# Performance work log

Measured on AMD Instinct MI355X. Metric: run time of the kernel, lower is better.

Reference implementation:

```python
import jax, jax.numpy as jnp
import numpy as np

LN_EPS = 1e-12


def layer_norm(x, g, b):
    mu = jnp.mean(x, axis=-1, keepdims=True)
    var = jnp.mean(jnp.square(x - mu), axis=-1, keepdims=True)
    return (x - mu) * jax.lax.rsqrt(var + LN_EPS) * g + b


def setup_inputs() -> dict:
    key = jax.random.key(0)
    ks = jax.random.split(key, 12)
    B, L, H, P, V = 8, 512, 768, 200, 30522
    src_scores = jax.random.normal(ks[0], (B, L, L), jnp.float32)
    seq_hidden = jax.random.normal(ks[1], (B, L, H), jnp.float32)
    seq_mask = jax.random.randint(ks[2], (B, L), 0, 2).astype(jnp.float32)
    pos_emb = jax.random.normal(ks[3], (512, P), jnp.float32) * 0.02
    Wp = jax.random.normal(ks[4], (H, P), jnp.float32) * 0.02
    bp = jnp.zeros((H,), jnp.float32)
    Wt = jax.random.normal(ks[5], (H, H), jnp.float32) * 0.02
    bt = jnp.zeros((H,), jnp.float32)
    ln_g = jnp.ones((H,), jnp.float32)
    ln_b = jnp.zeros((H,), jnp.float32)
    Wd = jax.random.normal(ks[6], (V, H), jnp.float32) * 0.02
    dec_bias = jnp.zeros((V,), jnp.float32)
    return dict(src_scores=src_scores, seq_hidden=seq_hidden, seq_mask=seq_mask,
                pos_emb=pos_emb, Wp=Wp, bp=bp, Wt=Wt, bt=bt,
                ln_g=ln_g, ln_b=ln_b, Wd=Wd, dec_bias=dec_bias)


def reference(src_scores, seq_hidden, seq_mask, pos_emb, Wp, bp, Wt, bt, ln_g, ln_b, Wd, dec_bias):
    L = src_scores.shape[1]
    # position embeddings for first L positions, projected to hidden size: [L, H]
    pos_h = pos_emb[:L] @ Wp.T + bp
    # pos_scores[b, l, s] = pos_h[l] . seq_hidden[b, s]
    pos_scores = jnp.einsum('lh,bsh->bls', pos_h, seq_hidden)
    scores = pos_scores + src_scores + seq_mask[:, None, :] * -10000.0
    alpha = jax.nn.softmax(scores, axis=-1)                 # [B, L, L]
    seq_sum = jnp.einsum('bls,bsh->blh', alpha, seq_hidden)  # [B, L, H]
    # BertPredictionHeadTransform: dense -> gelu (exact) -> LayerNorm
    h = layer_norm(jax.nn.gelu(seq_sum @ Wt.T + bt, approximate=False), ln_g, ln_b)
    target_scores = h @ Wd.T + dec_bias                      # [B, L, V]
    return target_scores
```

## Files before the change

### kernel.cpp

```cpp
#include <hip/hip_runtime.h>

using f32x4  = __attribute__((ext_vector_type(4))) float;
using short8 = __attribute__((ext_vector_type(8))) short;
using short4v= __attribute__((ext_vector_type(4))) short;
typedef __attribute__((ext_vector_type(8))) __bf16 bf16x8;

__device__ static inline short f2bf(float f){
    unsigned u = __builtin_bit_cast(unsigned, f);
    u += 0x7fffu + ((u >> 16) & 1u);
    return (short)(u >> 16);
}

__device__ static inline void gload_lds16(const void* g, void* l){
    __builtin_amdgcn_global_load_lds(
        (const __attribute__((address_space(1))) void*)g,
        (__attribute__((address_space(3))) void*)l, 16, 0, 0);
}

#define BARM() asm volatile("s_barrier" ::: "memory")

#define BKK 64

template<int EPI, bool T2D>
__global__ __launch_bounds__(256, 2)
void gemm_bt(const short* __restrict__ A, const short* __restrict__ B,
             float* __restrict__ outF, short* __restrict__ outB,
             const float* __restrict__ bias,
             const float* __restrict__ addmat, const float* __restrict__ mask,
             int K, int ldc, int Ncheck,
             long sA, long sB, long sC, long sX, int maskStride)
{
    __shared__ short Abuf[128*BKK];
    __shared__ short Bbuf[128*BKK];
    const int tid  = threadIdx.x;
    const int wave = tid >> 6;
    const int lane = tid & 63;
    const int bz   = blockIdx.z;

    int bx = blockIdx.x, by = blockIdx.y;
    if constexpr (T2D) {
        const int GX = gridDim.x, GY = gridDim.y;
        const int f  = blockIdx.y * GX + blockIdx.x;
        const int nfull  = GX >> 3;
        const int fullsz = (nfull << 3) * GY;
        int mg, mloc, nloc, nbase;
        if (f < fullsz) {
            const int band = f / (GY << 3);
            const int r    = f - band * (GY << 3);
            mg   = r >> 6;
            const int rr = r & 63;
            mloc = rr & 7; nloc = rr >> 3;
            nbase = band << 3;
        } else {
            const int rem = GX & 7;
            const int fp  = f - fullsz;
            const int gsz = rem << 3;
            mg   = fp / gsz;
            const int rr = fp - mg * gsz;
            mloc = rr & 7; nloc = rr >> 3;
            nbase = nfull << 3;
        }
        bx = nbase + nloc;
        by = (mg << 3) + mloc;
    }
    const int m0 = by * 128;
    const int n0 = bx * 128;
    const short* Ab = A + (long)bz * sA;
    const short* Bb = B + (long)bz * sB;

    const int wr = (wave >> 1) * 64;
    const int wc = (wave &  1) * 64;

    f32x4 acc[4][4];
    #pragma unroll
    for (int i=0;i<4;++i)
        #pragma unroll
        for (int j=0;j<4;++j) acc[i][j] = (f32x4){0.f,0.f,0.f,0.f};

    const int srow = wave*32 + (lane >> 3);
    const int kch  = (lane & 7) ^ (lane >> 3);
    const short* gA = Ab + (long)(m0 + srow)*K + kch*8;
    const short* gB = Bb + (long)(n0 + srow)*K + kch*8;
    short* lA = Abuf + wave*32*BKK;
    short* lB = Bbuf + wave*32*BKK;

    for (int k0 = 0; k0 < K; k0 += BKK) {
        __syncthreads();
        #pragma unroll
        for (int is=0; is<4; ++is){
            gload_lds16(gA + k0 + (long)is*8*K, lA + is*8*BKK);
            gload_lds16(gB + k0 + (long)is*8*K, lB + is*8*BKK);
        }
        __syncthreads();
        #pragma unroll
        for (int ks=0; ks<2; ++ks){
            bf16x8 af[4], bfr[4];
            const int chunk = ks*4 + (lane >> 4);
            #pragma unroll
            for (int mi=0;mi<4;++mi){
                int row = wr + mi*16 + (lane & 15);
                af[mi] = *(const bf16x8*)((const char*)Abuf + row*128 + ((chunk ^ (row & 7))<<4));
            }
            #pragma unroll
            for (int ni=0;ni<4;++ni){
                int row = wc + ni*16 + (lane & 15);
                bfr[ni] = *(const bf16x8*)((const char*)Bbuf + row*128 + ((chunk ^ (row & 7))<<4));
            }
            #pragma unroll
            for (int mi=0;mi<4;++mi)
                #pragma unroll
                for (int ni=0;ni<4;++ni)
                    acc[mi][ni] = __builtin_amdgcn_mfma_f32_16x16x32_bf16(af[mi], bfr[ni], acc[mi][ni], 0, 0, 0);
        }
    }

    const int rb = (lane >> 4) * 4;
    const int cb = lane & 15;
    #pragma unroll
    for (int mi=0;mi<4;++mi){
        #pragma unroll
        for (int r=0;r<4;++r){
            const int row = m0 + wr + mi*16 + rb + r;
            #pragma unroll
            for (int ni=0;ni<4;++ni){
                const int col = n0 + wc + ni*16 + cb;
                float v = acc[mi][ni][r];
                if constexpr (EPI == 0) {
                    v += addmat[(long)bz*sX + (long)row*ldc + col]
                         - 10000.f * mask[bz*maskStride + col];
                    outF[(long)bz*sC + (long)row*ldc + col] = v;
                } else if constexpr (EPI == 1) {
                    outB[(long)bz*sC + (long)row*ldc + col] = f2bf(v);
                } else if constexpr (EPI == 3) {
                    if (col < Ncheck) outF[(long)row*ldc + col] = v + bias[col];
                } else if constexpr (EPI == 4) {
                    outB[(long)row*ldc + col] = f2bf(v + bias[col]);
                }
            }
        }
    }
}

template<bool T2D>
__global__ __launch_bounds__(512, 1)
void gemm_bt256p(const short* __restrict__ A, const short* __restrict__ B,
                 float* __restrict__ outF, const float* __restrict__ bias,
                 int K, int ldc, int Ncheck, int maxBrow)
{
    __shared__ __align__(16) short Ab[2][2][256*32];
    __shared__ __align__(16) short Bb[2][2][256*32];
    const int tid  = threadIdx.x;
    const int wave = tid >> 6;
    const int lane = tid & 63;

    int bx = blockIdx.x, by = blockIdx.y;
    if constexpr (T2D) {
        const int GX = gridDim.x, GY = gridDim.y;
        const int f  = blockIdx.y * GX + blockIdx.x;
        const int band = f / (GY << 3);
        const int r2   = f - band * (GY << 3);
        const int mg   = r2 >> 6;
        const int rr   = r2 & 63;
        bx = (band << 3) + (rr >> 3);
        by = (mg << 3) + (rr & 7);
    }
    const int m0 = by * 256;
    const int n0 = bx * 256;

    const int wr = (wave >> 2) * 128;
    const int wc = (wave & 3) * 64;

    f32x4 acc[8][4];
    #pragma unroll
    for (int i=0;i<8;++i)
        #pragma unroll
        for (int j=0;j<4;++j) acc[i][j] = (f32x4){0.f,0.f,0.f,0.f};

    const int srow = wave*16 + (lane >> 2);
    const int cg   = (lane & 3) ^ ((lane >> 3) & 3);
    const short* gA0 = A + (long)(m0 + srow)       * K + cg*8;
    const short* gA1 = gA0 + (long)128 * K;
    int br0 = n0 + srow;        if (br0 > maxBrow) br0 = maxBrow;
    int br1 = n0 + 128 + srow;  if (br1 > maxBrow) br1 = maxBrow;
    const short* gB0 = B + (long)br0 * K + cg*8;
    const short* gB1 = B + (long)br1 * K + cg*8;
    const int so = wave*16*32;

    const int nt = K / 64;

    #define SA(bb,kh,kc) { gload_lds16(gA0 + (kc) + (kh)*32, &Ab[bb][kh][so]); \
                           gload_lds16(gA1 + (kc) + (kh)*32, &Ab[bb][kh][128*32 + so]); }
    #define SB(bb,kh,kc) { gload_lds16(gB0 + (kc) + (kh)*32, &Bb[bb][kh][so]); \
                           gload_lds16(gB1 + (kc) + (kh)*32, &Bb[bb][kh][128*32 + so]); }

    const int ch   = (lane >> 4) ^ ((lane >> 1) & 3);
    const int aoff = (wr + (lane & 15))*32 + ch*8;
    const int boff = (wc + (lane & 15))*32 + ch*8;

    SA(0,0,0); SB(0,0,0); SA(0,1,0); SB(0,1,0);
    asm volatile("s_waitcnt vmcnt(4)" ::: "memory");
    BARM();

    for (int t = 0; t < nt; ++t) {
        const int buf = t & 1, nb = buf ^ 1;
        const bool pf = (t + 1) < nt;
        const long kc = (long)(t + 1) * 64;
        bf16x8 af[8], bq[2];

        #define RDA(kh) { _Pragma("unroll") \
            for (int mi=0;mi<8;++mi) af[mi] = *(const bf16x8*)&Ab[buf][kh][aoff + mi*512]; }
        #define RDB(kh,n0i) { bq[0] = *(const bf16x8*)&Bb[buf][kh][boff + (n0i)*512]; \
                              bq[1] = *(const bf16x8*)&Bb[buf][kh][boff + (n0i+1)*512]; }
        #define MF(n0i) { __builtin_amdgcn_s_setprio(1); _Pragma("unroll") \
            for (int mi=0;mi<8;++mi){ \
                acc[mi][n0i]   = __builtin_amdgcn_mfma_f32_16x16x32_bf16(af[mi], bq[0], acc[mi][n0i],   0,0,0); \
                acc[mi][n0i+1] = __builtin_amdgcn_mfma_f32_16x16x32_bf16(af[mi], bq[1], acc[mi][n0i+1], 0,0,0); } \
            __builtin_amdgcn_s_setprio(0); }

        RDA(0); RDB(0,0);
        if (pf) SA(nb,0,kc);
        BARM();
        MF(0);
        BARM();
        RDB(0,2);
        if (pf) { SB(nb,0,kc); asm volatile("s_waitcnt vmcnt(4)" ::: "memory"); }
        else    {              asm volatile("s_waitcnt vmcnt(0)" ::: "memory"); }
        BARM();
        MF(2);
        BARM();
        RDA(1); RDB(1,0);
        if (pf) SA(nb,1,kc);
        BARM();
        MF(0);
        BARM();
        RDB(1,2);
        if (pf) { SB(nb,1,kc); asm volatile("s_waitcnt vmcnt(4)" ::: "memory"); }
        else    {              asm volatile("s_waitcnt vmcnt(0)" ::: "memory"); }
        BARM();
        MF(2);
        BARM();

        #undef RDA
        #undef RDB
        #undef MF
    }

    const int rb = (lane >> 4) * 4;
    const int cb = lane & 15;
    #pragma unroll
    for (int mi=0;mi<8;++mi){
        #pragma unroll
        for (int r=0;r<4;++r){
            const long row = (long)m0 + wr + mi*16 + rb + r;
            #pragma unroll
            for (int ni=0;ni<4;++ni){
                const int col = n0 + wc + ni*16 + cb;
                if (col < Ncheck)
                    outF[row*ldc + col] = acc[mi][ni][r] + bias[col];
            }
        }
    }
}

__global__ __launch_bounds__(256)
void conv_bf16(const float* __restrict__ in, short* __restrict__ out, long n, long ntot)
{
    const long stride = (long)gridDim.x * 2048;
    for (long i = ((long)blockIdx.x*256 + threadIdx.x)*8; i < ntot; i += stride){
        short8 o = (short8){0,0,0,0,0,0,0,0};
        if (i < n){
            f32x4 a = *(const f32x4*)(in + i);
            f32x4 b = *(const f32x4*)(in + i + 4);
            o[0]=f2bf(a[0]); o[1]=f2bf(a[1]); o[2]=f2bf(a[2]); o[3]=f2bf(a[3]);
            o[4]=f2bf(b[0]); o[5]=f2bf(b[1]); o[6]=f2bf(b[2]); o[7]=f2bf(b[3]);
        }
        *(short8*)(out + i) = o;
    }
}

__global__ __launch_bounds__(256)
void conv_pad(const float* __restrict__ in, short* __restrict__ out,
              int Cin, int Cpad, int total)
{
    int idx = blockIdx.x*256 + threadIdx.x;
    if (idx >= total) return;
    int r = idx / Cpad, c = idx - r*Cpad;
    short v = 0;
    if (c < Cin) v = f2bf(in[(long)r*Cin + c]);
    out[idx] = v;
}

__global__ __launch_bounds__(256)
void transpose_to_bf16(const float* __restrict__ in, short* __restrict__ out, int R, int C)
{
    __shared__ float t[32][33];
    const long boff = (long)blockIdx.z * R * C;
    const float* inb = in + boff;
    short* outb = out + boff;
    int c0 = blockIdx.x*32, r0 = blockIdx.y*32;
    int tx = threadIdx.x & 31, ty = threadIdx.x >> 5;
    #pragma unroll
    for (int j=0;j<32;j+=8) t[ty+j][tx] = inb[(long)(r0+ty+j)*C + c0+tx];
    __syncthreads();
    #pragma unroll
    for (int j=0;j<32;j+=8) outb[(long)(c0+ty+j)*R + r0+tx] = f2bf(t[tx][ty+j]);
}

__global__ __launch_bounds__(256)
void softmax_bf16(const float* __restrict__ scores, short* __restrict__ alpha, int L)
{
    const int row  = blockIdx.x*4 + (threadIdx.x >> 6);
    const int lane = threadIdx.x & 63;
    const float* p = scores + (long)row*L + lane*8;
    f32x4 v0 = *(const f32x4*)p;
    f32x4 v1 = *(const f32x4*)(p+4);
    float x[8] = {v0[0],v0[1],v0[2],v0[3],v1[0],v1[1],v1[2],v1[3]};
    float m = x[0];
    #pragma unroll
    for (int j=1;j<8;++j) m = fmaxf(m, x[j]);
    #pragma unroll
    for (int off=32; off; off>>=1) m = fmaxf(m, __shfl_xor(m, off));
    float s = 0.f;
    #pragma unroll
    for (int j=0;j<8;++j){ x[j] = __expf(x[j]-m); s += x[j]; }
    #pragma unroll
    for (int off=32; off; off>>=1) s += __shfl_xor(s, off);
    const float rinv = 1.f / s;
    short8 o;
    #pragma unroll
    for (int j=0;j<8;++j) o[j] = f2bf(x[j]*rinv);
    *(short8*)(alpha + (long)row*L + lane*8) = o;
}

__global__ __launch_bounds__(256)
void gelu_ln(const float* __restrict__ lin, short* __restrict__ h,
             const float* __restrict__ g, const float* __restrict__ b, int H)
{
    const int row  = blockIdx.x*4 + (threadIdx.x >> 6);
    const int lane = threadIdx.x & 63;
    const float* p = lin + (long)row*H;
    float x[12];
    #pragma unroll
    for (int c=0;c<3;++c){
        f32x4 v = *(const f32x4*)(p + c*256 + lane*4);
        x[c*4+0]=v[0]; x[c*4+1]=v[1]; x[c*4+2]=v[2]; x[c*4+3]=v[3];
    }
    float sum=0.f, sq=0.f;
    #pragma unroll
    for (int j=0;j<12;++j){
        float t = 0.5f * x[j] * (1.f + erff(x[j]*0.70710678118654752f));
        x[j] = t; sum += t; sq += t*t;
    }
    #pragma unroll
    for (int off=32; off; off>>=1){ sum += __shfl_xor(sum, off); sq += __shfl_xor(sq, off); }
    const float mu  = sum * (1.f/768.f);
    const float var = sq  * (1.f/768.f) - mu*mu;
    const float inv = rsqrtf(var + 1e-12f);
    #pragma unroll
    for (int c=0;c<3;++c){
        short4v o;
        #pragma unroll
        for (int j=0;j<4;++j){
            int col = c*256 + lane*4 + j;
            o[j] = f2bf((x[c*4+j]-mu)*inv*g[col] + b[col]);
        }
        *(short4v*)(h + (long)row*H + c*256 + lane*4) = o;
    }
}

extern "C" void kernel_launch(void* const* d_in, const int* in_sizes, int n_in,
                              void* d_out, int out_size, void* d_ws, size_t ws_size,
                              hipStream_t stream)
{
    const float* src_scores = (const float*)d_in[0];
    const float* seq_hidden = (const float*)d_in[1];
    const float* seq_mask   = (const float*)d_in[2];
    const float* pos_emb    = (const float*)d_in[3];
    const float* Wp         = (const float*)d_in[4];
    const float* bp         = (const float*)d_in[5];
    const float* Wt         = (const float*)d_in[6];
    const float* bt         = (const float*)d_in[7];
    const float* ln_g       = (const float*)d_in[8];
    const float* ln_b       = (const float*)d_in[9];
    const float* Wd         = (const float*)d_in[10];
    const float* dec_bias   = (const float*)d_in[11];
    float* out = (float*)d_out;

    const int B=8, L=512, H=768, V=30522, Vp=30592, Kp=256;

    const size_t need = ((size_t)Vp*H + (size_t)B*L*H) * sizeof(short);
    if (ws_size < need) return;
    short* wd_bf = (short*)d_ws;
    short* h_bf  = wd_bf + (long)Vp*H;

    char* sc = (char*)d_out;
    short* sh_nat = (short*)sc;  sc += (long)B*L*H*2;
    short* sh_t   = (short*)sc;  sc += (long)B*L*H*2;
    short* pe_p   = (short*)sc;  sc += (long)L*Kp*2;
    short* wp_p   = (short*)sc;  sc += (long)H*Kp*2;
    short* pos_h  = (short*)sc;  sc += (long)L*H*2;
    short* wt_bf  = (short*)sc;  sc += (long)H*H*2;
    float* scoresb= (float*)sc;  sc += (long)B*L*L*4;
    short* alpha  = (short*)sc;  sc += (long)B*L*L*2;
    short* seqsum = (short*)sc;  sc += (long)B*L*H*2;
    float* lin5   = (float*)sc;  sc += (long)B*L*H*4;

    {   long n=(long)V*H, ntot=(long)Vp*H;
        int blocks=(int)((ntot+2047)/2048); if (blocks>2048) blocks=2048;
        conv_bf16<<<dim3(blocks),256,0,stream>>>(Wd, wd_bf, n, ntot); }
    {   long n=(long)H*H; int blocks=(int)((n+2047)/2048);
        conv_bf16<<<dim3(blocks),256,0,stream>>>(Wt, wt_bf, n, n); }
    {   long n=(long)B*L*H; int blocks=(int)((n+2047)/2048); if (blocks>2048) blocks=2048;
        conv_bf16<<<dim3(blocks),256,0,stream>>>(seq_hidden, sh_nat, n, n); }
    transpose_to_bf16<<<dim3(H/32, L/32, B),256,0,stream>>>(seq_hidden, sh_t, L, H);
    {   int total=L*Kp;
        conv_pad<<<dim3((total+255)/256),256,0,stream>>>(pos_emb, pe_p, 200, Kp, total); }
    {   int total=H*Kp;
        conv_pad<<<dim3((total+255)/256),256,0,stream>>>(Wp, wp_p, 200, Kp, total); }

    gemm_bt<4,false><<<dim3(H/128, L/128, 1),256,0,stream>>>(
        pe_p, wp_p, nullptr, pos_h, bp, nullptr, nullptr,
        Kp, H, H, 0L, 0L, 0L, 0L, 0);

    gemm_bt<0,false><<<dim3(L/128, L/128, B),256,0,stream>>>(
        pos_h, sh_nat, scoresb, nullptr, nullptr, src_scores, seq_mask,
        H, L, L, 0L, (long)L*H, (long)L*L, (long)L*L, L);

    softmax_bf16<<<dim3(B*L/4),256,0,stream>>>(scoresb, alpha, L);

    gemm_bt<1,false><<<dim3(H/128, L/128, B),256,0,stream>>>(
        alpha, sh_t, nullptr, seqsum, nullptr, nullptr, nullptr,
        L, H, H, (long)L*L, (long)H*L, (long)L*H, 0L, 0);

    gemm_bt<3,false><<<dim3(H/128, (B*L)/128, 1),256,0,stream>>>(
        seqsum, wt_bf, lin5, nullptr, bt, nullptr, nullptr,
        H, H, H, 0L, 0L, 0L, 0L, 0);

    gelu_ln<<<dim3(B*L/4),256,0,stream>>>(lin5, h_bf, ln_g, ln_b, H);

    gemm_bt256p<true><<<dim3(120, 16), 512, 0, stream>>>(
        h_bf, wd_bf, out, dec_bias, H, V, V, Vp - 1);
}
```

Before: 481.8 us.

## Deepen decoder GEMM pipeline to four 32-wide K stages with prefetch distance three

The 256x256 decoder GEMM now keeps four single K=32 LDS stages in a ring instead of two double-buffered K=64 stages, and prefetches three iterations ahead. The vmcnt waits are adjusted so more global-to-LDS loads are in flight, which is meant to hide memory latency better behind the MFMA work. LDS use stays the same. Each iteration now does half the MFMA work per barrier pair, so barrier overhead relative to compute goes up.

```diff
diff --git a/kernel.cpp b/kernel.cpp
--- a/kernel.cpp
+++ b/kernel.cpp
@@ -143,12 +143,12 @@
 
 template<bool T2D>
 __global__ __launch_bounds__(512, 1)
-void gemm_bt256p(const short* __restrict__ A, const short* __restrict__ B,
+void gemm_bt256d(const short* __restrict__ A, const short* __restrict__ B,
                  float* __restrict__ outF, const float* __restrict__ bias,
                  int K, int ldc, int Ncheck, int maxBrow)
 {
-    __shared__ __align__(16) short Ab[2][2][256*32];
-    __shared__ __align__(16) short Bb[2][2][256*32];
+    __shared__ __align__(16) short Ab[4][256*32];
+    __shared__ __align__(16) short Bb[4][256*32];
     const int tid  = threadIdx.x;
     const int wave = tid >> 6;
     const int lane = tid & 63;
@@ -186,64 +186,64 @@
     const short* gB1 = B + (long)br1 * K + cg*8;
     const int so = wave*16*32;
 
-    const int nt = K / 64;
-
-    #define SA(bb,kh,kc) { gload_lds16(gA0 + (kc) + (kh)*32, &Ab[bb][kh][so]); \
-                           gload_lds16(gA1 + (kc) + (kh)*32, &Ab[bb][kh][128*32 + so]); }
-    #define SB(bb,kh,kc) { gload_lds16(gB0 + (kc) + (kh)*32, &Bb[bb][kh][so]); \
-                           gload_lds16(gB1 + (kc) + (kh)*32, &Bb[bb][kh][128*32 + so]); }
+    const int nt = K / 32;
+
+    #define SA(bb,t_) { gload_lds16(gA0 + (t_)*32, &Ab[bb][so]); \
+                        gload_lds16(gA1 + (t_)*32, &Ab[bb][128*32 + so]); }
+    #define SB(bb,t_) { gload_lds16(gB0 + (t_)*32, &Bb[bb][so]); \
+                        gload_lds16(gB1 + (t_)*32, &Bb[bb][128*32 + so]); }
 
     const int ch   = (lane >> 4) ^ ((lane >> 1) & 3);
     const int aoff = (wr + (lane & 15))*32 + ch*8;
     const int boff = (wc + (lane & 15))*32 + ch*8;
 
-    SA(0,0,0); SB(0,0,0); SA(0,1,0); SB(0,1,0);
-    asm volatile("s_waitcnt vmcnt(4)" ::: "memory");
+    SA(0,0); SB(0,0); SA(1,1); SB(1,1); SA(2,2); SB(2,2);
+    asm volatile("s_waitcnt vmcnt(8)" ::: "memory");
     BARM();
 
     for (int t = 0; t < nt; ++t) {
-        const int buf = t & 1, nb = buf ^ 1;
-        const bool pf = (t + 1) < nt;
-        const long kc = (long)(t + 1) * 64;
-        bf16x8 af[8], bq[2];
-
-        #define RDA(kh) { _Pragma("unroll") \
-            for (int mi=0;mi<8;++mi) af[mi] = *(const bf16x8*)&Ab[buf][kh][aoff + mi*512]; }
-        #define RDB(kh,n0i) { bq[0] = *(const bf16x8*)&Bb[buf][kh][boff + (n0i)*512]; \
-                              bq[1] = *(const bf16x8*)&Bb[buf][kh][boff + (n0i+1)*512]; }
-        #define MF(n0i) { __builtin_amdgcn_s_setprio(1); _Pragma("unroll") \
-            for (int mi=0;mi<8;++mi){ \
-                acc[mi][n0i]   = __builtin_amdgcn_mfma_f32_16x16x32_bf16(af[mi], bq[0], acc[mi][n0i],   0,0,0); \
-                acc[mi][n0i+1] = __builtin_amdgcn_mfma_f32_16x16x32_bf16(af[mi], bq[1], acc[mi][n0i+1], 0,0,0); } \
-            __builtin_amdgcn_s_setprio(0); }
-
-        RDA(0); RDB(0,0);
-        if (pf) SA(nb,0,kc);
+        const int buf = t & 3;
+        const int pb  = (t + 3) & 3;
+        const bool pf = (t + 3) < nt;
+        bf16x8 af[8], bq0, bq1;
+
+        #pragma unroll
+        for (int mi=0;mi<8;++mi) af[mi] = *(const bf16x8*)&Ab[buf][aoff + mi*512];
+        bq0 = *(const bf16x8*)&Bb[buf][boff];
+        bq1 = *(const bf16x8*)&Bb[buf][boff + 512];
+        if (pf) SA(pb, t+3);
         BARM();
-        MF(0);
+        __builtin_amdgcn_s_setprio(1);
+        #pragma unroll
+        for (int mi=0;mi<8;++mi){
+            acc[mi][0] = __builtin_amdgcn_mfma_f32_16x16x32_bf16(af[mi], bq0, acc[mi][0], 0,0,0);
+            acc[mi][1] = __builtin_amdgcn_mfma_f32_16x16x32_bf16(af[mi], bq1, acc[mi][1], 0,0,0);
+        }
+        __builtin_amdgcn_s_setprio(0);
         BARM();
-        RDB(0,2);
-        if (pf) { SB(nb,0,kc); asm volatile("s_waitcnt vmcnt(4)" ::: "memory"); }
-        else    {              asm volatile("s_waitcnt vmcnt(0)" ::: "memory"); }
+
+        bq0 = *(const bf16x8*)&Bb[buf][boff + 2*512];
+        bq1 = *(const bf16x8*)&Bb[buf][boff + 3*512];
+        if (pf) {
+            SB(pb, t+3);
+            asm volatile("s_waitcnt vmcnt(8)" ::: "memory");
+        } else if (t + 2 < nt) {
+            asm volatile("s_waitcnt vmcnt(4)" ::: "memory");
+        } else {
+            asm volatile("s_waitcnt vmcnt(0)" ::: "memory");
+        }
         BARM();
-        MF(2);
+        __builtin_amdgcn_s_setprio(1);
+        #pragma unroll
+        for (int mi=0;mi<8;++mi){
+            acc[mi][2] = __builtin_amdgcn_mfma_f32_16x16x32_bf16(af[mi], bq0, acc[mi][2], 0,0,0);
+            acc[mi][3] = __builtin_amdgcn_mfma_f32_16x16x32_bf16(af[mi], bq1, acc[mi][3], 0,0,0);
+        }
+        __builtin_amdgcn_s_setprio(0);
         BARM();
-        RDA(1); RDB(1,0);
-        if (pf) SA(nb,1,kc);
-        BARM();
-        MF(0);
-        BARM();
-        RDB(1,2);
-        if (pf) { SB(nb,1,kc); asm volatile("s_waitcnt vmcnt(4)" ::: "memory"); }
-        else    {              asm volatile("s_waitcnt vmcnt(0)" ::: "memory"); }
-        BARM();
-        MF(2);
-        BARM();
-
-        #undef RDA
-        #undef RDB
-        #undef MF
-    }
+    }
+    #undef SA
+    #undef SB
 
     const int rb = (lane >> 4) * 4;
     const int cb = lane & 15;
@@ -438,6 +438,6 @@
 
     gelu_ln<<<dim3(B*L/4),256,0,stream>>>(lin5, h_bf, ln_g, ln_b, H);
 
-    gemm_bt256p<true><<<dim3(120, 16), 512, 0, stream>>>(
+    gemm_bt256d<true><<<dim3(120, 16), 512, 0, stream>>>(
         h_bf, wd_bf, out, dec_bias, H, V, V, Vp - 1);
 }
```

Result: slower. 513.9 us (+6.7%).
